# Kernel tuning notes

Hardware: AMD Instinct MI355X
Metric: run time of the kernel (lower is better)

Reference implementation:

```python
import jax, jax.numpy as jnp
import numpy as np

N, E, HID, H, L = 50000, 100000, 128, 4, 3
C = HID          # out_channels per head (concat=True -> H*C = 512)
ED = 1           # edge_dim
HC = H * C


def setup_inputs() -> dict:
    key = jax.random.key(0)
    ks = jax.random.split(key, 20)
    s = 0.05
    w = lambda k, shape: (jax.random.normal(k, shape, jnp.float32) * s)
    inp = {
        'x': jax.random.normal(ks[0], (N, HID), jnp.float32),
        'edge_index': jax.random.randint(ks[1], (2, E), 0, N),
        'edge_attr': jax.random.normal(ks[2], (E, ED), jnp.float32),
        # per-layer stacked parameters (TransformerConv + proj + LayerNorm)
        'Wq': w(ks[3], (L, HID, HC)), 'bq': jnp.zeros((L, HC), jnp.float32),
        'Wk': w(ks[4], (L, HID, HC)), 'bk': jnp.zeros((L, HC), jnp.float32),
        'Wv': w(ks[5], (L, HID, HC)), 'bv': jnp.zeros((L, HC), jnp.float32),
        'We': w(ks[6], (L, ED, HC)),                       # lin_edge, bias=False
        'Wskip': w(ks[7], (L, HID, HC)), 'bskip': jnp.zeros((L, HC), jnp.float32),
        'Wproj': w(ks[8], (L, HC, HID)), 'bproj': jnp.zeros((L, HID), jnp.float32),
        'gamma': jnp.ones((L, HID), jnp.float32), 'beta': jnp.zeros((L, HID), jnp.float32),
    }
    return inp


def reference(x, edge_index, edge_attr, Wq, bq, Wk, bk, Wv, bv, We, Wskip, bskip,
              Wproj, bproj, gamma, beta):
    src, dst = edge_index[0], edge_index[1]
    scale = 1.0 / jnp.sqrt(jnp.asarray(C, x.dtype))
    for l in range(L):
        q = (x @ Wq[l] + bq[l]).reshape(N, H, C)
        k = (x @ Wk[l] + bk[l]).reshape(N, H, C)
        v = (x @ Wv[l] + bv[l]).reshape(N, H, C)
        e = (edge_attr @ We[l]).reshape(E, H, C)
        kj = k[src] + e                                   # [E,H,C]
        alpha = jnp.einsum('ehc,ehc->eh', q[dst], kj) * scale
        # segment softmax over destination nodes
        amax = jax.ops.segment_max(alpha, dst, num_segments=N)
        p = jnp.exp(alpha - amax[dst])
        denom = jax.ops.segment_sum(p, dst, num_segments=N)
        a = p / (denom[dst] + 1e-16)                      # [E,H]
        msg = (v[src] + e) * a[:, :, None]                # [E,H,C]
        agg = jax.ops.segment_sum(msg, dst, num_segments=N).reshape(N, HC)
        conv = agg + x @ Wskip[l] + bskip[l]              # root/skip connection
        h = jax.nn.elu(conv @ Wproj[l] + bproj[l])        # proj + ELU (dropout=eval noop)
        y = x + h                                         # residual
        mu = jnp.mean(y, axis=-1, keepdims=True)
        var = jnp.var(y, axis=-1, keepdims=True)
        x = (y - mu) / jnp.sqrt(var + 1e-5) * gamma[l] + beta[l]
    return x
```

## Files before the change

kernel.cpp:

```cpp
#include <hip/hip_runtime.h>

#define NN 50000
#define NPAD 50176
#define EE 100000
#define HIDD 128
#define HH 4
#define CCC 128
#define HCC 512
#define QS 2048
#define LLL 3
#define SCALE 0.08838834764831845f

typedef unsigned short u16;
typedef unsigned int u32;
typedef __attribute__((ext_vector_type(8))) short bfrag;
typedef __attribute__((ext_vector_type(4))) float fx4;

__device__ __forceinline__ float bfl(u32 u){ return __uint_as_float(u << 16); }
__device__ __forceinline__ float bfh(u32 u){ return __uint_as_float(u & 0xffff0000u); }
__device__ __forceinline__ u16 f2bf(float f){
  u32 u = __float_as_uint(f);
  return (u16)((u + 0x7fffu + ((u >> 16) & 1u)) >> 16);
}
__device__ __forceinline__ u32 pack2(float a, float b){
  return (u32)f2bf(a) | ((u32)f2bf(b) << 16);
}

union bfcvt { bfrag f; uint4 u; };

#if defined(__has_builtin)
#if __has_builtin(__builtin_amdgcn_global_load_lds)
#define USE_GLL 1
#endif
#endif
#ifndef USE_GLL
#define USE_GLL 0
#endif

__device__ __forceinline__ void gll16(const u16* g, u16* l){
#if USE_GLL
  __builtin_amdgcn_global_load_lds(
      (const __attribute__((address_space(1))) unsigned int*)(const void*)g,
      (__attribute__((address_space(3))) unsigned int*)(void*)l, 16, 0, 0);
#else
  uint4 v = *(const uint4*)g;
  *(uint4*)l = v;
#endif
}

__global__ __launch_bounds__(256) void kzero(int* p, int n){
  int i = blockIdx.x * 256 + threadIdx.x;
  if (i < n) p[i] = 0;
}

__global__ __launch_bounds__(256) void kcvt(const float* __restrict__ x,
                                            u16* __restrict__ xb){
  int i = blockIdx.x * 256 + threadIdx.x;
  if (i >= NPAD*HIDD/4) return;
  int base = i * 4;
  uint2 o = make_uint2(0u, 0u);
  if (base < NN*HIDD) {
    float4 v = *(const float4*)(x + base);
    o = make_uint2(pack2(v.x,v.y), pack2(v.z,v.w));
  }
  *(uint2*)(xb + base) = o;
}

__global__ __launch_bounds__(256) void khist(const int* __restrict__ ei, int* __restrict__ counts){
  int e = blockIdx.x * 256 + threadIdx.x;
  if (e < EE) atomicAdd(&counts[ei[EE + e]], 1);
}

__global__ __launch_bounds__(256) void kscanA(const int* __restrict__ counts, int* __restrict__ bsum){
  __shared__ int sh[256];
  int t = threadIdx.x, i = blockIdx.x * 256 + t;
  sh[t] = (i < NN) ? counts[i] : 0;
  __syncthreads();
  #pragma unroll
  for (int off = 128; off; off >>= 1) {
    if (t < off) sh[t] += sh[t + off];
    __syncthreads();
  }
  if (t == 0) bsum[blockIdx.x] = sh[0];
}

__global__ __launch_bounds__(256) void kscanB(int* __restrict__ bsum, int nb){
  __shared__ int sh[256];
  int t = threadIdx.x;
  int v = (t < nb) ? bsum[t] : 0;
  sh[t] = v;
  __syncthreads();
  #pragma unroll
  for (int off = 1; off < 256; off <<= 1) {
    int a = (t >= off) ? sh[t - off] : 0;
    __syncthreads();
    sh[t] += a;
    __syncthreads();
  }
  if (t < nb) bsum[t] = sh[t] - v;
}

__global__ __launch_bounds__(256) void kscanC(const int* __restrict__ counts,
                                              const int* __restrict__ bsum,
                                              int* __restrict__ rowptr){
  __shared__ int sh[256];
  int t = threadIdx.x, i = blockIdx.x * 256 + t;
  int v = (i < NN) ? counts[i] : 0;
  sh[t] = v;
  __syncthreads();
  #pragma unroll
  for (int off = 1; off < 256; off <<= 1) {
    int a = (t >= off) ? sh[t - off] : 0;
    __syncthreads();
    sh[t] += a;
    __syncthreads();
  }
  if (i <= NN) rowptr[i] = bsum[blockIdx.x] + sh[t] - v;
}

__global__ __launch_bounds__(256) void kscatter(const int* __restrict__ ei,
                                                const float* __restrict__ ea,
                                                const int* __restrict__ rowptr,
                                                int* __restrict__ fill,
                                                int* __restrict__ csr_src,
                                                float* __restrict__ csr_ea){
  int e = blockIdx.x * 256 + threadIdx.x;
  if (e >= EE) return;
  int d = ei[EE + e];
  int pos = rowptr[d] + atomicAdd(&fill[d], 1);
  csr_src[pos] = ei[e];
  csr_ea[pos]  = ea[e];
}

__global__ __launch_bounds__(256) void kprep(
    const float* __restrict__ Wq, const float* __restrict__ Wk,
    const float* __restrict__ Wv,
    const float* __restrict__ bq, const float* __restrict__ bk,
    const float* __restrict__ bv,
    const float* __restrict__ Wp,
    u16* __restrict__ Wt, u16* __restrict__ Wpt, float* __restrict__ bias_cat)
{
  int id = blockIdx.x * 256 + threadIdx.x;
  if (id < 1536*128) {
    int n = id >> 7, k = id & 127;
    int m = n >> 9, nc = n & 511;
    const float* W = (m==0)?Wq:(m==1)?Wk:Wv;
    Wt[id] = f2bf(W[(size_t)k*HCC + nc]);
  } else if (id < 1536*128 + 128*512) {
    int j = id - 1536*128;
    int n = j >> 9, k = j & 511;
    Wpt[j] = f2bf(Wp[(size_t)k*HIDD + n]);
  } else if (id < 1536*128 + 128*512 + 1536) {
    int n = id - (1536*128 + 128*512);
    int m = n >> 9, nc = n & 511;
    const float* b = (m==0)?bq:(m==1)?bk:bv;
    bias_cat[n] = b[nc];
  }
}

__global__ __launch_bounds__(256) void kskp2(
    const float* __restrict__ Wsk, const u16* __restrict__ Wpt,
    u16* __restrict__ Wskt)
{
  const int t = threadIdx.x;
  const int wave = t >> 6, lane = t & 63;
  const int lo = lane & 15, hi = lane >> 4;
  const int wr = wave >> 1, wc = wave & 1;
  const int b0 = blockIdx.x * 64 + wr * 32;
  const int a0 = blockIdx.y * 32 + wc * 16;

  fx4 acc[2] = {};
  #pragma unroll
  for (int kk = 0; kk < 16; ++kk) {
    const float* wp = Wsk + (size_t)(a0 + lo)*HCC + kk*32 + hi*8;
    float4 u = *(const float4*)(wp);
    float4 w = *(const float4*)(wp + 4);
    bfcvt bc;
    bc.u = make_uint4(pack2(u.x,u.y), pack2(u.z,u.w),
                      pack2(w.x,w.y), pack2(w.z,w.w));
    #pragma unroll
    for (int fr = 0; fr < 2; ++fr) {
      bfrag af = *(const bfrag*)(Wpt + (size_t)(b0 + fr*16 + lo)*HCC + kk*32 + hi*8);
      acc[fr] = __builtin_amdgcn_mfma_f32_16x16x32_bf16(af, bc.f, acc[fr], 0, 0, 0);
    }
  }
  #pragma unroll
  for (int fr = 0; fr < 2; ++fr)
    #pragma unroll
    for (int j = 0; j < 4; ++j)
      Wskt[(size_t)(b0 + fr*16 + hi*4 + j)*128 + a0 + lo] = f2bf(acc[fr][j]);
}

__global__ __launch_bounds__(256) void kbpe(
    const float* __restrict__ bsk, const float* __restrict__ Wp,
    const float* __restrict__ bp, float* __restrict__ bpe)
{
  __shared__ float part[8][32];
  const int c = blockIdx.x * 32 + (threadIdx.x & 31);
  const int seg = threadIdx.x >> 5;
  float s = 0.f;
  #pragma unroll
  for (int j = 0; j < 64; ++j)
    s += bsk[seg*64 + j] * Wp[(size_t)(seg*64 + j)*HIDD + c];
  part[seg][threadIdx.x & 31] = s;
  __syncthreads();
  if (seg == 0) {
    float tot = bp[c];
    #pragma unroll
    for (int k = 0; k < 8; ++k) tot += part[k][threadIdx.x & 31];
    bpe[c] = tot;
  }
}

__global__ __launch_bounds__(256) void k1_mfma(
    const u16* __restrict__ xb, const u16* __restrict__ Wt,
    const float* __restrict__ bias, u16* __restrict__ qkvs)
{
  __shared__ u16 lds[16896];
  const int t = threadIdx.x;
  const int wave = t >> 6, lane = t & 63;
  const int lo = lane & 15, hi = lane >> 4;
  const int wr = wave >> 1, wc = wave & 1;

  int b = blockIdx.x;
  const int qq = 4692/8, rr = 4692%8;
  int xcd = b & 7, slot = b >> 3;
  int wgid = (xcd < rr ? xcd*(qq+1) : rr*(qq+1) + (xcd-rr)*qq) + slot;
  const int rb = (wgid / 12) * 128;
  const int cb = (wgid % 12) * 128;

  auto STAGE = [&](int buf, int kk){
    #pragma unroll
    for (int half = 0; half < 2; ++half) {
      int c = wave*64 + lane + half*256;
      int row = c >> 2, seg = c & 3;
      gll16(xb + (size_t)(rb + row)*HIDD + kk*32 + seg*8,
            &lds[buf*4096 + (wave*64 + half*256)*8]);
    }
    #pragma unroll
    for (int half = 0; half < 2; ++half) {
      int c = wave*64 + lane + half*256;
      int row = c >> 2, seg = c & 3;
      gll16(Wt + (size_t)(cb + row)*HIDD + kk*32 + seg*8,
            &lds[8192 + buf*4096 + (wave*64 + half*256)*8]);
    }
  };

#if !USE_GLL
  auto STAGE_REG = [&](int buf, int kk){
    #pragma unroll
    for (int half = 0; half < 2; ++half) {
      int c = wave*64 + lane + half*256;
      int row = c >> 2, seg = c & 3;
      uint4 v = *(const uint4*)(xb + (size_t)(rb + row)*HIDD + kk*32 + seg*8);
      *(uint4*)&lds[buf*4096 + c*8] = v;
      uint4 w = *(const uint4*)(Wt + (size_t)(cb + row)*HIDD + kk*32 + seg*8);
      *(uint4*)&lds[8192 + buf*4096 + c*8] = w;
    }
  };
#define DO_STAGE STAGE_REG
#else
#define DO_STAGE STAGE
#endif

  fx4 acc[4][4] = {};

  DO_STAGE(0, 0);
  __syncthreads();
  #pragma unroll
  for (int kk = 0; kk < 4; ++kk) {
    const int buf = kk & 1;
    if (kk < 3) DO_STAGE(buf ^ 1, kk + 1);
    bfrag a[4], b2[4];
    #pragma unroll
    for (int fr = 0; fr < 4; ++fr)
      a[fr] = *(const bfrag*)&lds[buf*4096 + (wr*64 + fr*16 + lo)*32 + hi*8];
    #pragma unroll
    for (int fc = 0; fc < 4; ++fc)
      b2[fc] = *(const bfrag*)&lds[8192 + buf*4096 + (wc*64 + fc*16 + lo)*32 + hi*8];
    #pragma unroll
    for (int fr = 0; fr < 4; ++fr)
      #pragma unroll
      for (int fc = 0; fc < 4; ++fc)
        acc[fr][fc] = __builtin_amdgcn_mfma_f32_16x16x32_bf16(a[fr], b2[fc], acc[fr][fc], 0, 0, 0);
    __syncthreads();
  }

  float bb[4];
  #pragma unroll
  for (int fc = 0; fc < 4; ++fc) bb[fc] = bias[cb + wc*64 + fc*16 + lo];
  #pragma unroll
  for (int fr = 0; fr < 4; ++fr)
    #pragma unroll
    for (int fc = 0; fc < 4; ++fc)
      #pragma unroll
      for (int j = 0; j < 4; ++j)
        lds[(size_t)(wr*64 + fr*16 + hi*4 + j)*132 + wc*64 + fc*16 + lo]
            = f2bf(acc[fr][fc][j] + bb[fc]);
  __syncthreads();

  #pragma unroll
  for (int i = 0; i < 8; ++i) {
    int f = t + 256*i;
    int row = f >> 4, seg = f & 15;
    if (rb + row < NN)
      *(uint4*)(qkvs + (size_t)(rb+row)*QS + cb + seg*8) = *(uint4*)&lds[(size_t)row*132 + seg*8];
  }
}

__global__ __launch_bounds__(256) void k23_fused(
    u16* __restrict__ qkvs, const int* __restrict__ rowptr,
    const int* __restrict__ csr_src, const float* __restrict__ csr_ea,
    const float* __restrict__ We)
{
  int wave = threadIdx.x >> 6, lane = threadIdx.x & 63;
  int n = blockIdx.x * 4 + wave;
  if (n >= NN) return;
  int h = lane >> 4, c0 = (lane & 15) * 8;

  uint4 qa = *(const uint4*)(qkvs + (size_t)n*QS + h*CCC + c0);
  float qf[8] = {bfl(qa.x),bfh(qa.x),bfl(qa.y),bfh(qa.y),
                 bfl(qa.z),bfh(qa.z),bfl(qa.w),bfh(qa.w)};
  float4 w0 = *(const float4*)(We + h*CCC + c0);
  float4 w1 = *(const float4*)(We + h*CCC + c0 + 4);
  float wf[8] = {w0.x,w0.y,w0.z,w0.w,w1.x,w1.y,w1.z,w1.w};

  float qw = qf[0]*wf[0]+qf[1]*wf[1]+qf[2]*wf[2]+qf[3]*wf[3]
           + qf[4]*wf[4]+qf[5]*wf[5]+qf[6]*wf[6]+qf[7]*wf[7];
  #pragma unroll
  for (int off = 8; off; off >>= 1) qw += __shfl_xor(qw, off);

  int beg = rowptr[n], end = rowptr[n+1];
  float accv[8] = {};
  float accp = 0.f, accw = 0.f;

  for (int i = beg; i < end; ++i) {
    int src = csr_src[i];
    float eav = csr_ea[i];
    uint4 ka = *(const uint4*)(qkvs + (size_t)src*QS + 512 + h*CCC + c0);
    float s = qf[0]*bfl(ka.x) + qf[1]*bfh(ka.x)
            + qf[2]*bfl(ka.y) + qf[3]*bfh(ka.y)
            + qf[4]*bfl(ka.z) + qf[5]*bfh(ka.z)
            + qf[6]*bfl(ka.w) + qf[7]*bfh(ka.w);
    #pragma unroll
    for (int off = 8; off; off >>= 1) s += __shfl_xor(s, off);
    float p = expf((s + eav * qw) * SCALE);
    uint4 va = *(const uint4*)(qkvs + (size_t)src*QS + 1024 + h*CCC + c0);
    accv[0] += p*bfl(va.x); accv[1] += p*bfh(va.x);
    accv[2] += p*bfl(va.y); accv[3] += p*bfh(va.y);
    accv[4] += p*bfl(va.z); accv[5] += p*bfh(va.z);
    accv[6] += p*bfl(va.w); accv[7] += p*bfh(va.w);
    accp += p; accw += p*eav;
  }

  float inv = 1.f / (accp + 1e-16f);
  float se  = accw * inv;
  u16* ap = qkvs + (size_t)n*QS + 1536 + h*CCC + c0;
  *(uint4*)ap = make_uint4(
    pack2(accv[0]*inv+se*wf[0], accv[1]*inv+se*wf[1]),
    pack2(accv[2]*inv+se*wf[2], accv[3]*inv+se*wf[3]),
    pack2(accv[4]*inv+se*wf[4], accv[5]*inv+se*wf[5]),
    pack2(accv[6]*inv+se*wf[6], accv[7]*inv+se*wf[7]));
}

__global__ __launch_bounds__(256) void k4_mfma(
    const u16* __restrict__ qkvs, const u16* __restrict__ xb_in,
    const u16* __restrict__ Wpt, const u16* __restrict__ Wskt,
    const float* __restrict__ bpe,
    const float* __restrict__ gamma, const float* __restrict__ beta,
    const float* x_in, float* x_out, u16* __restrict__ xb_out)
{
  __shared__ __align__(16) unsigned char ldsraw[34816];
  u16*   lds = (u16*)ldsraw;
  float* yt  = (float*)ldsraw;
  float* mu_s = (float*)(ldsraw + 33792);
  float* rs_s = (float*)(ldsraw + 34048);
  const int t = threadIdx.x;
  const int wave = t >> 6, lane = t & 63;
  const int lo = lane & 15, hi = lane >> 4;
  const int wr = wave >> 1, wc = wave & 1;
  const int rb = blockIdx.x * 64;

  auto STAGE = [&](int buf, int kk){
    {
      int c = wave*64 + lane;
      int row = c >> 2, seg = c & 3;
      const u16* src = (kk < 16)
        ? qkvs + (size_t)(rb + row)*QS + 1536 + kk*32 + seg*8
        : xb_in + (size_t)(rb + row)*HIDD + (kk-16)*32 + seg*8;
#if USE_GLL
      gll16(src, &lds[buf*2048 + (wave*64)*8]);
#else
      *(uint4*)&lds[buf*2048 + c*8] = *(const uint4*)src;
#endif
    }
    #pragma unroll
    for (int half = 0; half < 2; ++half) {
      int c = wave*64 + lane + half*256;
      int col = c >> 2, seg = c & 3;
      const u16* src = (kk < 16)
        ? Wpt  + (size_t)col*512 + kk*32 + seg*8
        : Wskt + (size_t)col*128 + (kk-16)*32 + seg*8;
#if USE_GLL
      gll16(src, &lds[4096 + buf*4096 + (wave*64 + half*256)*8]);
#else
      *(uint4*)&lds[4096 + buf*4096 + c*8] = *(const uint4*)src;
#endif
    }
  };

  fx4 acc[2][4] = {};

  STAGE(0, 0);
  __syncthreads();
  #pragma unroll
  for (int kk = 0; kk < 20; ++kk) {
    const int buf = kk & 1;
    if (kk < 19) STAGE(buf ^ 1, kk + 1);
    bfrag a[2], b[4];
    #pragma unroll
    for (int fr = 0; fr < 2; ++fr)
      a[fr] = *(const bfrag*)&lds[buf*2048 + (wr*32 + fr*16 + lo)*32 + hi*8];
    #pragma unroll
    for (int fc = 0; fc < 4; ++fc)
      b[fc] = *(const bfrag*)&lds[4096 + buf*4096 + (wc*64 + fc*16 + lo)*32 + hi*8];
    #pragma unroll
    for (int fr = 0; fr < 2; ++fr)
      #pragma unroll
      for (int fc = 0; fc < 4; ++fc)
        acc[fr][fc] = __builtin_amdgcn_mfma_f32_16x16x32_bf16(a[fr], b[fc], acc[fr][fc], 0, 0, 0);
    __syncthreads();
  }

  #pragma unroll
  for (int fr = 0; fr < 2; ++fr)
    #pragma unroll
    for (int fc = 0; fc < 4; ++fc) {
      int col = wc*64 + fc*16 + lo;
      float bb = bpe[col];
      #pragma unroll
      for (int j = 0; j < 4; ++j) {
        int r = wr*32 + fr*16 + hi*4 + j;
        int row = rb + r;
        float v = acc[fr][fc][j] + bb;
        v = v > 0.f ? v : expm1f(v);
        float xv = (row < NN) ? x_in[(size_t)row*HIDD + col] : 0.f;
        yt[(size_t)r*132 + col] = xv + v;
      }
    }
  __syncthreads();

  {
    int r = t >> 2, seg = t & 3;
    float s = 0.f, s2 = 0.f;
    #pragma unroll
    for (int j = 0; j < 32; ++j) {
      float y = yt[(size_t)r*132 + seg*32 + j];
      s += y; s2 += y*y;
    }
    s += __shfl_xor(s, 1); s2 += __shfl_xor(s2, 1);
    s += __shfl_xor(s, 2); s2 += __shfl_xor(s2, 2);
    if (seg == 0) {
      float mu = s * (1.f/128.f);
      float var = s2 * (1.f/128.f) - mu*mu;
      mu_s[r] = mu;
      rs_s[r] = rsqrtf(var + 1e-5f);
    }
  }
  __syncthreads();

  #pragma unroll
  for (int i = 0; i < 8; ++i) {
    int f = t + 256*i;
    int r = f >> 5, c4 = (f & 31) * 4;
    int row = rb + r;
    if (row >= NN) continue;
    float mu = mu_s[r], rs = rs_s[r];
    float4 g  = *(const float4*)(gamma + c4);
    float4 bt = *(const float4*)(beta + c4);
    float4 yv = *(float4*)&yt[(size_t)r*132 + c4];
    float4 o = make_float4((yv.x-mu)*rs*g.x + bt.x, (yv.y-mu)*rs*g.y + bt.y,
                           (yv.z-mu)*rs*g.z + bt.z, (yv.w-mu)*rs*g.w + bt.w);
    *(float4*)(x_out + (size_t)row*HIDD + c4) = o;
    *(uint2*)(xb_out + (size_t)row*HIDD + c4) = make_uint2(pack2(o.x,o.y), pack2(o.z,o.w));
  }
}

extern "C" void kernel_launch(void* const* d_in, const int* in_sizes, int n_in,
                              void* d_out, int out_size, void* d_ws, size_t ws_size,
                              hipStream_t stream)
{
  const float* x    = (const float*)d_in[0];
  const int*   ei   = (const int*)d_in[1];
  const float* ea   = (const float*)d_in[2];
  const float* Wq   = (const float*)d_in[3];
  const float* bq   = (const float*)d_in[4];
  const float* Wk   = (const float*)d_in[5];
  const float* bk   = (const float*)d_in[6];
  const float* Wv   = (const float*)d_in[7];
  const float* bv   = (const float*)d_in[8];
  const float* We   = (const float*)d_in[9];
  const float* Wsk  = (const float*)d_in[10];
  const float* bsk  = (const float*)d_in[11];
  const float* Wp   = (const float*)d_in[12];
  const float* bp   = (const float*)d_in[13];
  const float* gamma= (const float*)d_in[14];
  const float* beta = (const float*)d_in[15];

  char* wsb = (char*)d_ws;
  size_t off = 0;
  auto alloc = [&](size_t bytes) -> void* {
    void* p = wsb + off;
    off += (bytes + 255) & ~(size_t)255;
    return p;
  };
  u16*   qkvs    = (u16*)  alloc((size_t)NPAD*QS*2);
  u16*   xb      = (u16*)  alloc((size_t)NPAD*HIDD*2);
  int*   rowptr  = (int*)  alloc((size_t)(NN+1)*4);
  int*   counts  = (int*)  alloc((size_t)NN*4);
  int*   fill    = (int*)  alloc((size_t)NN*4);
  int*   bsum    = (int*)  alloc((size_t)256*4);
  int*   csr_src = (int*)  alloc((size_t)EE*4);
  float* csr_ea  = (float*)alloc((size_t)EE*4);
  u16*   Wt      = (u16*)  alloc((size_t)1536*128*2);
  u16*   Wpt     = (u16*)  alloc((size_t)128*512*2);
  u16*   Wskt    = (u16*)  alloc((size_t)128*128*2);
  float* biasc   = (float*)alloc((size_t)1536*4);
  float* bpe     = (float*)alloc((size_t)128*4);
  float* xio     = (float*)d_out;

  const int gn  = (NN + 255)/256;
  const int ge  = (EE + 255)/256;
  const int gp  = (1536*128 + 128*512 + 1536 + 255)/256;
  const int gc  = (NPAD*HIDD/4 + 255)/256;
  const int g1  = 12 * ((NN + 127)/128);
  const dim3 gsk(2, 4);
  const int g23 = (NN + 3)/4;
  const int g4  = NPAD/64;

  kzero<<<gn, 256, 0, stream>>>(counts, NN);
  kzero<<<gn, 256, 0, stream>>>(fill, NN);
  khist<<<ge, 256, 0, stream>>>(ei, counts);
  kscanA<<<gn, 256, 0, stream>>>(counts, bsum);
  kscanB<<<1, 256, 0, stream>>>(bsum, gn);
  kscanC<<<gn, 256, 0, stream>>>(counts, bsum, rowptr);
  kscatter<<<ge, 256, 0, stream>>>(ei, ea, rowptr, fill, csr_src, csr_ea);
  kcvt<<<gc, 256, 0, stream>>>(x, xb);

  for (int l = 0; l < LLL; ++l) {
    const float* Wq_l  = Wq  + (size_t)l*HIDD*HCC;
    const float* Wk_l  = Wk  + (size_t)l*HIDD*HCC;
    const float* Wv_l  = Wv  + (size_t)l*HIDD*HCC;
    const float* Wsk_l = Wsk + (size_t)l*HIDD*HCC;
    const float* bq_l  = bq  + (size_t)l*HCC;
    const float* bk_l  = bk  + (size_t)l*HCC;
    const float* bv_l  = bv  + (size_t)l*HCC;
    const float* bsk_l = bsk + (size_t)l*HCC;
    const float* We_l  = We  + (size_t)l*HCC;
    const float* Wp_l  = Wp  + (size_t)l*HCC*HIDD;
    const float* bp_l  = bp  + (size_t)l*HIDD;
    const float* g_l   = gamma + (size_t)l*HIDD;
    const float* b_l   = beta  + (size_t)l*HIDD;

    const float* xin = (l == 0) ? x : xio;

    kprep<<<gp, 256, 0, stream>>>(Wq_l, Wk_l, Wv_l, bq_l, bk_l, bv_l,
                                  Wp_l, Wt, Wpt, biasc);
    kskp2<<<gsk, 256, 0, stream>>>(Wsk_l, Wpt, Wskt);
    kbpe<<<4, 256, 0, stream>>>(bsk_l, Wp_l, bp_l, bpe);
    k1_mfma<<<g1, 256, 0, stream>>>(xb, Wt, biasc, qkvs);
    k23_fused<<<g23, 256, 0, stream>>>(qkvs, rowptr, csr_src, csr_ea, We_l);
    k4_mfma<<<g4, 256, 0, stream>>>(qkvs, xb, Wpt, Wskt, bpe, g_l, b_l, xin, xio, xb);
  }
}
```

Measured before the change: 451.3 us.

## Do LayerNorm epilogue in registers, read bf16 residual, write fp32 only on last layer

The projection kernel's epilogue now keeps the ELU+residual values in registers. It computes the LayerNorm row statistics with wave shuffles plus a tiny shared-memory exchange, instead of staging a full fp32 tile in LDS. The residual is read from the bf16 copy of x rather than the fp32 buffer, and the fp32 output is written only on the last layer, which cuts global traffic and LDS use. In exchange, the residual carries bf16 rounding error into every layer. The final stores also become scalar 2-byte and 4-byte writes instead of vectorised ones.

```diff
diff --git a/kernel.cpp b/kernel.cpp
--- a/kernel.cpp
+++ b/kernel.cpp
@@ -18,6 +18,7 @@
 
 __device__ __forceinline__ float bfl(u32 u){ return __uint_as_float(u << 16); }
 __device__ __forceinline__ float bfh(u32 u){ return __uint_as_float(u & 0xffff0000u); }
+__device__ __forceinline__ float bf1(u16 u){ return __uint_as_float((u32)u << 16); }
 __device__ __forceinline__ u16 f2bf(float f){
   u32 u = __float_as_uint(f);
   return (u16)((u + 0x7fffu + ((u >> 16) & 1u)) >> 16);
@@ -368,13 +369,10 @@
     const u16* __restrict__ Wpt, const u16* __restrict__ Wskt,
     const float* __restrict__ bpe,
     const float* __restrict__ gamma, const float* __restrict__ beta,
-    const float* x_in, float* x_out, u16* __restrict__ xb_out)
-{
-  __shared__ __align__(16) unsigned char ldsraw[34816];
-  u16*   lds = (u16*)ldsraw;
-  float* yt  = (float*)ldsraw;
-  float* mu_s = (float*)(ldsraw + 33792);
-  float* rs_s = (float*)(ldsraw + 34048);
+    float* __restrict__ x_out, u16* __restrict__ xb_out, int last)
+{
+  __shared__ u16 lds[12288];
+  __shared__ float ps[64][2], ps2[64][2];
   const int t = threadIdx.x;
   const int wave = t >> 6, lane = t & 63;
   const int lo = lane & 15, hi = lane >> 4;
@@ -432,58 +430,59 @@
     __syncthreads();
   }
 
-  #pragma unroll
-  for (int fr = 0; fr < 2; ++fr)
-    #pragma unroll
-    for (int fc = 0; fc < 4; ++fc) {
-      int col = wc*64 + fc*16 + lo;
-      float bb = bpe[col];
+  float y[2][4][4];
+  #pragma unroll
+  for (int fc = 0; fc < 4; ++fc) {
+    int col = wc*64 + fc*16 + lo;
+    float bb = bpe[col];
+    #pragma unroll
+    for (int fr = 0; fr < 2; ++fr)
       #pragma unroll
       for (int j = 0; j < 4; ++j) {
-        int r = wr*32 + fr*16 + hi*4 + j;
-        int row = rb + r;
+        int row = rb + wr*32 + fr*16 + hi*4 + j;
         float v = acc[fr][fc][j] + bb;
         v = v > 0.f ? v : expm1f(v);
-        float xv = (row < NN) ? x_in[(size_t)row*HIDD + col] : 0.f;
-        yt[(size_t)r*132 + col] = xv + v;
+        float xv = (row < NN) ? bf1(xb_in[(size_t)row*HIDD + col]) : 0.f;
+        y[fr][fc][j] = xv + v;
       }
-    }
-  __syncthreads();
-
-  {
-    int r = t >> 2, seg = t & 3;
-    float s = 0.f, s2 = 0.f;
-    #pragma unroll
-    for (int j = 0; j < 32; ++j) {
-      float y = yt[(size_t)r*132 + seg*32 + j];
-      s += y; s2 += y*y;
-    }
-    s += __shfl_xor(s, 1); s2 += __shfl_xor(s2, 1);
-    s += __shfl_xor(s, 2); s2 += __shfl_xor(s2, 2);
-    if (seg == 0) {
+  }
+
+  #pragma unroll
+  for (int fr = 0; fr < 2; ++fr)
+    #pragma unroll
+    for (int j = 0; j < 4; ++j) {
+      float s  = y[fr][0][j] + y[fr][1][j] + y[fr][2][j] + y[fr][3][j];
+      float s2 = y[fr][0][j]*y[fr][0][j] + y[fr][1][j]*y[fr][1][j]
+               + y[fr][2][j]*y[fr][2][j] + y[fr][3][j]*y[fr][3][j];
+      #pragma unroll
+      for (int off = 8; off; off >>= 1) { s += __shfl_xor(s, off); s2 += __shfl_xor(s2, off); }
+      if (lo == 0) {
+        int r = wr*32 + fr*16 + hi*4 + j;
+        ps[r][wc] = s; ps2[r][wc] = s2;
+      }
+    }
+  __syncthreads();
+
+  #pragma unroll
+  for (int fr = 0; fr < 2; ++fr)
+    #pragma unroll
+    for (int j = 0; j < 4; ++j) {
+      int r = wr*32 + fr*16 + hi*4 + j;
+      int row = rb + r;
+      if (row >= NN) continue;
+      float s  = ps[r][0] + ps[r][1];
+      float s2 = ps2[r][0] + ps2[r][1];
       float mu = s * (1.f/128.f);
       float var = s2 * (1.f/128.f) - mu*mu;
-      mu_s[r] = mu;
-      rs_s[r] = rsqrtf(var + 1e-5f);
-    }
-  }
-  __syncthreads();
-
-  #pragma unroll
-  for (int i = 0; i < 8; ++i) {
-    int f = t + 256*i;
-    int r = f >> 5, c4 = (f & 31) * 4;
-    int row = rb + r;
-    if (row >= NN) continue;
-    float mu = mu_s[r], rs = rs_s[r];
-    float4 g  = *(const float4*)(gamma + c4);
-    float4 bt = *(const float4*)(beta + c4);
-    float4 yv = *(float4*)&yt[(size_t)r*132 + c4];
-    float4 o = make_float4((yv.x-mu)*rs*g.x + bt.x, (yv.y-mu)*rs*g.y + bt.y,
-                           (yv.z-mu)*rs*g.z + bt.z, (yv.w-mu)*rs*g.w + bt.w);
-    *(float4*)(x_out + (size_t)row*HIDD + c4) = o;
-    *(uint2*)(xb_out + (size_t)row*HIDD + c4) = make_uint2(pack2(o.x,o.y), pack2(o.z,o.w));
-  }
+      float rs = rsqrtf(var + 1e-5f);
+      #pragma unroll
+      for (int fc = 0; fc < 4; ++fc) {
+        int col = wc*64 + fc*16 + lo;
+        float o = (y[fr][fc][j] - mu)*rs*gamma[col] + beta[col];
+        xb_out[(size_t)row*HIDD + col] = f2bf(o);
+        if (last) x_out[(size_t)row*HIDD + col] = o;
+      }
+    }
 }
 
 extern "C" void kernel_launch(void* const* d_in, const int* in_sizes, int n_in,
@@ -562,14 +561,13 @@
     const float* g_l   = gamma + (size_t)l*HIDD;
     const float* b_l   = beta  + (size_t)l*HIDD;
 
-    const float* xin = (l == 0) ? x : xio;
-
     kprep<<<gp, 256, 0, stream>>>(Wq_l, Wk_l, Wv_l, bq_l, bk_l, bv_l,
                                   Wp_l, Wt, Wpt, biasc);
     kskp2<<<gsk, 256, 0, stream>>>(Wsk_l, Wpt, Wskt);
     kbpe<<<4, 256, 0, stream>>>(bsk_l, Wp_l, bp_l, bpe);
     k1_mfma<<<g1, 256, 0, stream>>>(xb, Wt, biasc, qkvs);
     k23_fused<<<g23, 256, 0, stream>>>(qkvs, rowptr, csr_src, csr_ea, We_l);
-    k4_mfma<<<g4, 256, 0, stream>>>(qkvs, xb, Wpt, Wskt, bpe, g_l, b_l, xin, xio, xb);
-  }
-}
+    k4_mfma<<<g4, 256, 0, stream>>>(qkvs, xb, Wpt, Wskt, bpe, g_l, b_l,
+                                    xio, xb, (l == LLL-1) ? 1 : 0);
+  }
+}
```

New measurement: 494.7 us. +9.6%, slower.

## Halve k4 row tile, read residual from bf16, write fp32 output only last layer

Applied to the files above, without the earlier changes.

The projection/LayerNorm kernel now processes 32 rows per block instead of 64, doubling the grid and shrinking LDS for better occupancy. The residual input is read from the bf16 copy of x rather than the fp32 buffer. The fp32 output is stored only on the final layer, which removes redundant fp32 traffic. The bf16 residual lowers precision and the accumulated rounding error may affect tolerance.

```diff
diff --git a/kernel.cpp b/kernel.cpp
--- a/kernel.cpp
+++ b/kernel.cpp
@@ -18,6 +18,7 @@
 
 __device__ __forceinline__ float bfl(u32 u){ return __uint_as_float(u << 16); }
 __device__ __forceinline__ float bfh(u32 u){ return __uint_as_float(u & 0xffff0000u); }
+__device__ __forceinline__ float bf1(u16 u){ return __uint_as_float((u32)u << 16); }
 __device__ __forceinline__ u16 f2bf(float f){
   u32 u = __float_as_uint(f);
   return (u16)((u + 0x7fffu + ((u >> 16) & 1u)) >> 16);
@@ -368,30 +369,29 @@
     const u16* __restrict__ Wpt, const u16* __restrict__ Wskt,
     const float* __restrict__ bpe,
     const float* __restrict__ gamma, const float* __restrict__ beta,
-    const float* x_in, float* x_out, u16* __restrict__ xb_out)
-{
-  __shared__ __align__(16) unsigned char ldsraw[34816];
-  u16*   lds = (u16*)ldsraw;
-  float* yt  = (float*)ldsraw;
-  float* mu_s = (float*)(ldsraw + 33792);
-  float* rs_s = (float*)(ldsraw + 34048);
+    float* __restrict__ x_out, u16* __restrict__ xb_out, int last)
+{
+  __shared__ __align__(16) u16 lds[10240];
+  float* yt   = (float*)lds;
+  float* mu_s = (float*)&lds[8448];
+  float* rs_s = (float*)&lds[8512];
   const int t = threadIdx.x;
   const int wave = t >> 6, lane = t & 63;
   const int lo = lane & 15, hi = lane >> 4;
   const int wr = wave >> 1, wc = wave & 1;
-  const int rb = blockIdx.x * 64;
+  const int rb = blockIdx.x * 32;
 
   auto STAGE = [&](int buf, int kk){
-    {
+    if (wave < 2) {
       int c = wave*64 + lane;
       int row = c >> 2, seg = c & 3;
       const u16* src = (kk < 16)
         ? qkvs + (size_t)(rb + row)*QS + 1536 + kk*32 + seg*8
         : xb_in + (size_t)(rb + row)*HIDD + (kk-16)*32 + seg*8;
 #if USE_GLL
-      gll16(src, &lds[buf*2048 + (wave*64)*8]);
+      gll16(src, &lds[buf*1024 + (wave*64)*8]);
 #else
-      *(uint4*)&lds[buf*2048 + c*8] = *(const uint4*)src;
+      *(uint4*)&lds[buf*1024 + c*8] = *(const uint4*)src;
 #endif
     }
     #pragma unroll
@@ -402,14 +402,14 @@
         ? Wpt  + (size_t)col*512 + kk*32 + seg*8
         : Wskt + (size_t)col*128 + (kk-16)*32 + seg*8;
 #if USE_GLL
-      gll16(src, &lds[4096 + buf*4096 + (wave*64 + half*256)*8]);
+      gll16(src, &lds[2048 + buf*4096 + (wave*64 + half*256)*8]);
 #else
-      *(uint4*)&lds[4096 + buf*4096 + c*8] = *(const uint4*)src;
+      *(uint4*)&lds[2048 + buf*4096 + c*8] = *(const uint4*)src;
 #endif
     }
   };
 
-  fx4 acc[2][4] = {};
+  fx4 acc[4] = {};
 
   STAGE(0, 0);
   __syncthreads();
@@ -417,49 +417,48 @@
   for (int kk = 0; kk < 20; ++kk) {
     const int buf = kk & 1;
     if (kk < 19) STAGE(buf ^ 1, kk + 1);
-    bfrag a[2], b[4];
-    #pragma unroll
-    for (int fr = 0; fr < 2; ++fr)
-      a[fr] = *(const bfrag*)&lds[buf*2048 + (wr*32 + fr*16 + lo)*32 + hi*8];
+    bfrag a = *(const bfrag*)&lds[buf*1024 + (wr*16 + lo)*32 + hi*8];
+    bfrag b[4];
     #pragma unroll
     for (int fc = 0; fc < 4; ++fc)
-      b[fc] = *(const bfrag*)&lds[4096 + buf*4096 + (wc*64 + fc*16 + lo)*32 + hi*8];
-    #pragma unroll
-    for (int fr = 0; fr < 2; ++fr)
-      #pragma unroll
-      for (int fc = 0; fc < 4; ++fc)
-        acc[fr][fc] = __builtin_amdgcn_mfma_f32_16x16x32_bf16(a[fr], b[fc], acc[fr][fc], 0, 0, 0);
-    __syncthreads();
-  }
-
-  #pragma unroll
-  for (int fr = 0; fr < 2; ++fr)
-    #pragma unroll
-    for (int fc = 0; fc < 4; ++fc) {
-      int col = wc*64 + fc*16 + lo;
-      float bb = bpe[col];
-      #pragma unroll
-      for (int j = 0; j < 4; ++j) {
-        int r = wr*32 + fr*16 + hi*4 + j;
-        int row = rb + r;
-        float v = acc[fr][fc][j] + bb;
-        v = v > 0.f ? v : expm1f(v);
-        float xv = (row < NN) ? x_in[(size_t)row*HIDD + col] : 0.f;
-        yt[(size_t)r*132 + col] = xv + v;
-      }
-    }
+      b[fc] = *(const bfrag*)&lds[2048 + buf*4096 + (wc*64 + fc*16 + lo)*32 + hi*8];
+    #pragma unroll
+    for (int fc = 0; fc < 4; ++fc)
+      acc[fc] = __builtin_amdgcn_mfma_f32_16x16x32_bf16(a, b[fc], acc[fc], 0, 0, 0);
+    __syncthreads();
+  }
+
+  float y[4][4];
+  #pragma unroll
+  for (int fc = 0; fc < 4; ++fc) {
+    int col = wc*64 + fc*16 + lo;
+    float bb = bpe[col];
+    #pragma unroll
+    for (int j = 0; j < 4; ++j) {
+      int row = rb + wr*16 + hi*4 + j;
+      float v = acc[fc][j] + bb;
+      v = v > 0.f ? v : expm1f(v);
+      float xv = (row < NN) ? bf1(xb_in[(size_t)row*HIDD + col]) : 0.f;
+      y[fc][j] = xv + v;
+    }
+  }
+  #pragma unroll
+  for (int fc = 0; fc < 4; ++fc)
+    #pragma unroll
+    for (int j = 0; j < 4; ++j)
+      yt[(size_t)(wr*16 + hi*4 + j)*132 + wc*64 + fc*16 + lo] = y[fc][j];
   __syncthreads();
 
   {
-    int r = t >> 2, seg = t & 3;
+    int r = t >> 3, seg = t & 7;
     float s = 0.f, s2 = 0.f;
     #pragma unroll
-    for (int j = 0; j < 32; ++j) {
-      float y = yt[(size_t)r*132 + seg*32 + j];
-      s += y; s2 += y*y;
-    }
-    s += __shfl_xor(s, 1); s2 += __shfl_xor(s2, 1);
-    s += __shfl_xor(s, 2); s2 += __shfl_xor(s2, 2);
+    for (int j = 0; j < 16; ++j) {
+      float v = yt[(size_t)r*132 + seg*16 + j];
+      s += v; s2 += v*v;
+    }
+    #pragma unroll
+    for (int off = 4; off; off >>= 1) { s += __shfl_xor(s, off); s2 += __shfl_xor(s2, off); }
     if (seg == 0) {
       float mu = s * (1.f/128.f);
       float var = s2 * (1.f/128.f) - mu*mu;
@@ -470,7 +469,7 @@
   __syncthreads();
 
   #pragma unroll
-  for (int i = 0; i < 8; ++i) {
+  for (int i = 0; i < 4; ++i) {
     int f = t + 256*i;
     int r = f >> 5, c4 = (f & 31) * 4;
     int row = rb + r;
@@ -481,8 +480,8 @@
     float4 yv = *(float4*)&yt[(size_t)r*132 + c4];
     float4 o = make_float4((yv.x-mu)*rs*g.x + bt.x, (yv.y-mu)*rs*g.y + bt.y,
                            (yv.z-mu)*rs*g.z + bt.z, (yv.w-mu)*rs*g.w + bt.w);
-    *(float4*)(x_out + (size_t)row*HIDD + c4) = o;
     *(uint2*)(xb_out + (size_t)row*HIDD + c4) = make_uint2(pack2(o.x,o.y), pack2(o.z,o.w));
+    if (last) *(float4*)(x_out + (size_t)row*HIDD + c4) = o;
   }
 }
 
@@ -536,7 +535,7 @@
   const int g1  = 12 * ((NN + 127)/128);
   const dim3 gsk(2, 4);
   const int g23 = (NN + 3)/4;
-  const int g4  = NPAD/64;
+  const int g4  = NPAD/32;
 
   kzero<<<gn, 256, 0, stream>>>(counts, NN);
   kzero<<<gn, 256, 0, stream>>>(fill, NN);
@@ -562,14 +561,13 @@
     const float* g_l   = gamma + (size_t)l*HIDD;
     const float* b_l   = beta  + (size_t)l*HIDD;
 
-    const float* xin = (l == 0) ? x : xio;
-
     kprep<<<gp, 256, 0, stream>>>(Wq_l, Wk_l, Wv_l, bq_l, bk_l, bv_l,
                                   Wp_l, Wt, Wpt, biasc);
     kskp2<<<gsk, 256, 0, stream>>>(Wsk_l, Wpt, Wskt);
     kbpe<<<4, 256, 0, stream>>>(bsk_l, Wp_l, bp_l, bpe);
     k1_mfma<<<g1, 256, 0, stream>>>(xb, Wt, biasc, qkvs);
     k23_fused<<<g23, 256, 0, stream>>>(qkvs, rowptr, csr_src, csr_ea, We_l);
-    k4_mfma<<<g4, 256, 0, stream>>>(qkvs, xb, Wpt, Wskt, bpe, g_l, b_l, xin, xio, xb);
-  }
-}
+    k4_mfma<<<g4, 256, 0, stream>>>(qkvs, xb, Wpt, Wskt, bpe, g_l, b_l,
+                                    xio, xb, (l == LLL-1) ? 1 : 0);
+  }
+}
```

Result: no change. 446.1 us (-1.2%).
